# Kernel tuning notes

Hardware: AMD Instinct MI355X
Metric: run time of the kernel (lower is better)

## Reference

```python
import jax, jax.numpy as jnp
import numpy as np

N_NODE = 50000
N_EDGE = 800000
NODE_DIM, EDGE_DIM = 3, 4


def _relu(x):
    return jnp.maximum(x, 0)


def setup_inputs() -> dict:
    key = jax.random.key(0)
    ks = jax.random.split(key, 32)
    ki = iter(range(32))

    def w(shape):
        fan = shape[0]
        return (jax.random.normal(ks[next(ki)], shape, jnp.float32) / np.float32(np.sqrt(fan)))

    def b(n):
        return jnp.zeros((n,), jnp.float32)

    inp = {
        'nodes': jax.random.normal(ks[next(ki)], (N_NODE, NODE_DIM), jnp.float32),
        'edges': jax.random.normal(ks[next(ki)], (N_EDGE, EDGE_DIM), jnp.float32),
        'senders': jax.random.randint(ks[next(ki)], (N_EDGE,), 0, N_NODE, jnp.int32),
        'receivers': jax.random.randint(ks[next(ki)], (N_EDGE,), 0, N_NODE, jnp.int32),
        # psi1 encoder: [10 -> 256 -> 256 -> 128], relu after every layer (act_final=True)
        'mw0': w((NODE_DIM * 2 + EDGE_DIM, 256)), 'mb0': b(256),
        'mw1': w((256, 256)), 'mb1': b(256),
        'mw2': w((256, 128)), 'mb2': b(128),
        # psi2 attention: [128 -> 128 -> 128 -> 1], no final act
        'aw0': w((128, 128)), 'ab0': b(128),
        'aw1': w((128, 128)), 'ab1': b(128),
        'aw2': w((128, 1)), 'ab2': b(1),
        # psi3 value: [128 -> 256 -> 128], relu after every layer
        'vw0': w((128, 256)), 'vb0': b(256),
        'vw1': w((256, 128)), 'vb1': b(128),
        # psi4 decoder: [128 -> 256 -> 256 -> 1], no final act
        'uw0': w((128, 256)), 'ub0': b(256),
        'uw1': w((256, 256)), 'ub1': b(256),
        'uw2': w((256, 1)), 'ub2': b(1),
    }
    return inp


def reference(nodes, edges, senders, receivers,
              mw0, mb0, mw1, mb1, mw2, mb2,
              aw0, ab0, aw1, ab1, aw2, ab2,
              vw0, vb0, vw1, vb1,
              uw0, ub0, uw1, ub1, uw2, ub2):
    n_node = nodes.shape[0]
    # gather endpoint features and concat with edge features: (E, 2*node_dim+edge_dim)
    z = jnp.concatenate([nodes[senders], nodes[receivers], edges], axis=-1)
    # psi1 encoder (act_final=True)
    q = _relu(_relu(_relu(z @ mw0 + mb0) @ mw1 + mb1) @ mw2 + mb2)  # (E,128)
    # psi2 attention logits (no final act)
    w = (_relu(_relu(q @ aw0 + ab0) @ aw1 + ab1) @ aw2 + ab2)[:, 0]  # (E,)
    # segment softmax over receivers (matches torch scatter_reduce amax with -1e9 init)
    m = jax.ops.segment_max(w, receivers, num_segments=n_node)
    m = jnp.maximum(m, jnp.float32(-1e9))
    ex = jnp.exp(w - m[receivers])
    s = jax.ops.segment_sum(ex, receivers, num_segments=n_node)
    attn = ex / (s[receivers] + 1e-12)  # (E,)
    # psi3 value (act_final=True)
    v = _relu(_relu(q @ vw0 + vb0) @ vw1 + vb1)  # (E,128)
    # attention-weighted scatter-add aggregation to receiver nodes
    aggr = jax.ops.segment_sum(attn[:, None] * v, receivers, num_segments=n_node)  # (N,128)
    # psi4 decoder (no final act)
    out = _relu(_relu(aggr @ uw0 + ub0) @ uw1 + ub1) @ uw2 + ub2  # (N,1)
    return out
```

## Files before the change

kernel.cpp:

```cpp
#include <hip/hip_runtime.h>
#include <stdint.h>

#define NN_NODE 50000
#define NN_EDGE 800000

typedef _Float16 f16;
typedef _Float16 f16x2 __attribute__((ext_vector_type(2)));
typedef _Float16 f16x4 __attribute__((ext_vector_type(4)));
typedef _Float16 f16x8 __attribute__((ext_vector_type(8)));
typedef float f32x4 __attribute__((ext_vector_type(4)));

#define WT_MW0   0
#define WT_MW1   8192
#define WT_MW2   73728
#define WT_AW0   106496
#define WT_AW1   122880
#define WT_VW0   139264
#define WT_VW1   172032
#define WT_UW0   204800
#define WT_UW1   237568
#define WT_TOTAL 303104

#define V_OFF      606208ull
#define WL_OFF     205406208ull
#define CNT_OFF    208606208ull
#define BASE_OFF   208806208ull
#define AGGR_OFF   209006208ull

__device__ __forceinline__ int swz(int row, int col) {
    return row * 256 + ((((col >> 3) ^ (row & 7))) << 3) + (col & 7);
}

template<int K, int N, int KN, int EPI>
__device__ __forceinline__ void mlayer(const f16* in, int inoff,
        const f16* __restrict__ wt, const float* __restrict__ bias,
        f16* out, int outoff,
        f16x8* bf0, const f16* __restrict__ wtn, f16x8* bfn,
        const float* __restrict__ aw2, float* lpart,
        f16* __restrict__ vout, const int* sposp, int tid)
{
    const int wave = tid >> 6;
    const int lane = tid & 63;
    const int l15  = lane & 15;
    const int quad = lane >> 4;
    constexpr int NKS  = K >> 5;
    constexpr int NKH  = (NKS > 4) ? 4 : NKS;
    constexpr int NH   = NKS / NKH;
    constexpr int NCT  = N >> 4;
    constexpr int ITC  = NCT / 4;
    constexpr int NKNH = (KN >= 128) ? 4 : (KN >> 5);

    f32x4 acc[ITC][4];
#pragma unroll
    for (int i = 0; i < ITC; ++i)
#pragma unroll
        for (int ms = 0; ms < 4; ++ms)
            acc[i][ms] = (f32x4){0.f, 0.f, 0.f, 0.f};

    int sposv[4];
    if constexpr (EPI == 2) {
#pragma unroll
        for (int ms = 0; ms < 4; ++ms) sposv[ms] = sposp[ms * 16 + l15];
    }

    f16x8 bfl[2][NKH];

#pragma unroll
    for (int h = 0; h < NH; ++h) {
        if (h == 0) {
#pragma unroll
            for (int ks = 0; ks < NKH; ++ks) bfl[0][ks] = bf0[ks];
        } else {
            const f16* wrow = wt + (size_t)(wave * 16 + l15) * K + h * NKH * 32 + quad * 8;
#pragma unroll
            for (int ks = 0; ks < NKH; ++ks)
                bfl[0][ks] = *(const f16x8*)(wrow + ks * 32);
        }

        f16x8 af[4][NKH];
#pragma unroll
        for (int ms = 0; ms < 4; ++ms)
#pragma unroll
            for (int ks = 0; ks < NKH; ++ks)
                af[ms][ks] = *(const f16x8*)(in + swz(ms * 16 + l15,
                                    inoff + (h * NKH + ks) * 32 + quad * 8));
#pragma unroll
        for (int ms = 0; ms < 4; ++ms)
#pragma unroll
            for (int ks = 0; ks < NKH; ++ks)
                asm volatile("" : "+v"(af[ms][ks]));

        if constexpr (KN > 0) {
            if (h == NH - 1) {
                const f16* wrow = wtn + (size_t)(wave * 16 + l15) * KN + quad * 8;
#pragma unroll
                for (int ks = 0; ks < NKNH; ++ks)
                    bfn[ks] = *(const f16x8*)(wrow + ks * 32);
            }
        }

#pragma unroll
        for (int i = 0; i < ITC; ++i) {
            const int ct = wave + i * 4;
            if (i + 1 < ITC) {
                const f16* wrow2 = wt + (size_t)((ct + 4) * 16 + l15) * K + h * NKH * 32 + quad * 8;
#pragma unroll
                for (int ks = 0; ks < NKH; ++ks)
                    bfl[(i + 1) & 1][ks] = *(const f16x8*)(wrow2 + ks * 32);
            }
#pragma unroll
            for (int ms = 0; ms < 4; ++ms)
#pragma unroll
                for (int ks = 0; ks < NKH; ++ks)
                    acc[i][ms] = __builtin_amdgcn_mfma_f32_16x16x32_f16(
                        bfl[i & 1][ks], af[ms][ks], acc[i][ms], 0, 0, 0);
        }
    }

    float preg[4];
    if constexpr (EPI == 1) {
#pragma unroll
        for (int ms = 0; ms < 4; ++ms) preg[ms] = 0.f;
    }
#pragma unroll
    for (int i = 0; i < ITC; ++i) {
        const int ct = wave + i * 4;
        const int f0 = ct * 16 + quad * 4;
        const float4 bv = *(const float4*)(bias + f0);
        float4 awv;
        if constexpr (EPI == 1) awv = *(const float4*)(aw2 + f0);
#pragma unroll
        for (int ms = 0; ms < 4; ++ms) {
            if constexpr (EPI == 0) {
                f16x4 o;
                o[0] = (f16)fmaxf(acc[i][ms][0] + bv.x, 0.f);
                o[1] = (f16)fmaxf(acc[i][ms][1] + bv.y, 0.f);
                o[2] = (f16)fmaxf(acc[i][ms][2] + bv.z, 0.f);
                o[3] = (f16)fmaxf(acc[i][ms][3] + bv.w, 0.f);
                *(f16x4*)(out + swz(ms * 16 + l15, outoff + f0)) = o;
            } else if constexpr (EPI == 1) {
                preg[ms] += fmaxf(acc[i][ms][0] + bv.x, 0.f) * awv.x
                          + fmaxf(acc[i][ms][1] + bv.y, 0.f) * awv.y
                          + fmaxf(acc[i][ms][2] + bv.z, 0.f) * awv.z
                          + fmaxf(acc[i][ms][3] + bv.w, 0.f) * awv.w;
            } else {
                f16x4 o;
                o[0] = (f16)fmaxf(acc[i][ms][0] + bv.x, 0.f);
                o[1] = (f16)fmaxf(acc[i][ms][1] + bv.y, 0.f);
                o[2] = (f16)fmaxf(acc[i][ms][2] + bv.z, 0.f);
                o[3] = (f16)fmaxf(acc[i][ms][3] + bv.w, 0.f);
                *(f16x4*)(vout + (size_t)sposv[ms] * 128 + f0) = o;
            }
        }
    }
    if constexpr (EPI == 1) {
#pragma unroll
        for (int ms = 0; ms < 4; ++ms) {
            float r = preg[ms];
            r += __shfl_xor(r, 16);
            r += __shfl_xor(r, 32);
            if (quad == 0) lpart[wave * 64 + ms * 16 + l15] = r;
        }
    }
}

template<int K, int N>
__device__ __forceinline__ void mfma_layer_basic(const f16* in, int inoff,
        const f16* __restrict__ wt, const float* __restrict__ bias,
        f16* out, int outoff, int tid)
{
    const int wave = tid >> 6;
    const int lane = tid & 63;
    const int l15  = lane & 15;
    const int quad = lane >> 4;
    constexpr int NCT = N >> 4;
    constexpr int NKS = K >> 5;
    f16x8 af[4][NKS];
#pragma unroll
    for (int ms = 0; ms < 4; ++ms)
#pragma unroll
        for (int ks = 0; ks < NKS; ++ks)
            af[ms][ks] = *(const f16x8*)(in + swz(ms * 16 + l15, inoff + ks * 32 + quad * 8));
#pragma unroll 1
    for (int ct = wave; ct < NCT; ct += 4) {
        f16x8 bf[NKS];
        const f16* wrow = wt + (size_t)(ct * 16 + l15) * K + quad * 8;
#pragma unroll
        for (int ks = 0; ks < NKS; ++ks) bf[ks] = *(const f16x8*)(wrow + ks * 32);
        const int f0 = ct * 16 + quad * 4;
        const float4 bv = *(const float4*)(bias + f0);
#pragma unroll
        for (int ms = 0; ms < 4; ++ms) {
            f32x4 acc = {0.f, 0.f, 0.f, 0.f};
#pragma unroll
            for (int ks = 0; ks < NKS; ++ks)
                acc = __builtin_amdgcn_mfma_f32_16x16x32_f16(bf[ks], af[ms][ks], acc, 0, 0, 0);
            f16x4 o;
            o[0] = (f16)fmaxf(acc[0] + bv.x, 0.f);
            o[1] = (f16)fmaxf(acc[1] + bv.y, 0.f);
            o[2] = (f16)fmaxf(acc[2] + bv.z, 0.f);
            o[3] = (f16)fmaxf(acc[3] + bv.w, 0.f);
            *(f16x4*)(out + swz(ms * 16 + l15, outoff + f0)) = o;
        }
    }
}

struct WSeg { const float* src; int K, N, Kpad, dstOff; };
struct WSegs { WSeg s[9]; };

__global__ void prep_kernel(WSegs segs, f16* __restrict__ wt) {
    int idx = blockIdx.x * 256 + threadIdx.x;
    if (idx >= WT_TOTAL) return;
    int off = idx;
#pragma unroll
    for (int i = 0; i < 9; ++i) {
        int sz = segs.s[i].N * segs.s[i].Kpad;
        if (off < sz) {
            int n = off / segs.s[i].Kpad;
            int k = off - n * segs.s[i].Kpad;
            f16 val = (f16)0.f;
            if (k < segs.s[i].K) val = (f16)segs.s[i].src[k * segs.s[i].N + n];
            wt[segs.s[i].dstOff + off] = val;
            return;
        }
        off -= sz;
    }
}

__global__ void hist_kernel(const int* __restrict__ receivers, int* __restrict__ cnt) {
    int e = blockIdx.x * 256 + threadIdx.x;
    atomicAdd(&cnt[receivers[e]], 1);
}

__global__ __launch_bounds__(1024) void scan_kernel(int* __restrict__ cnt, int* __restrict__ base) {
    __shared__ int psum[1024];
    const int tid = threadIdx.x;
    const int CH = (NN_NODE + 1023) / 1024;
    const int lo = tid * CH;
    const int hi = min(lo + CH, NN_NODE);
    int s = 0;
    for (int i = lo; i < hi; ++i) s += cnt[i];
    psum[tid] = s;
    __syncthreads();
    for (int d = 1; d < 1024; d <<= 1) {
        int v = (tid >= d) ? psum[tid - d] : 0;
        __syncthreads();
        psum[tid] += v;
        __syncthreads();
    }
    int run = psum[tid] - s;
    for (int i = lo; i < hi; ++i) {
        int c = cnt[i];
        base[i] = run;
        cnt[i] = run;
        run += c;
    }
}

__global__ __launch_bounds__(256, 2) void edge_kernel(
        const float* __restrict__ nodes, const float* __restrict__ edges,
        const int* __restrict__ senders, const int* __restrict__ receivers,
        const f16* __restrict__ wt,
        const float* __restrict__ mb0, const float* __restrict__ mb1, const float* __restrict__ mb2,
        const float* __restrict__ ab0, const float* __restrict__ ab1,
        const float* __restrict__ aw2, const float* __restrict__ ab2,
        const float* __restrict__ vb0, const float* __restrict__ vb1,
        f16* __restrict__ vout, float* __restrict__ wlog, int* __restrict__ cursor)
{
    __shared__ f16 ldsbuf[2 * 64 * 256];
    __shared__ int spos[64];
    __shared__ float lpart[256];
    f16* bufA = ldsbuf;
    f16* bufB = ldsbuf + 64 * 256;
    const int tid = threadIdx.x;
    const int e0 = blockIdx.x * 64;
    const int wave = tid >> 6;
    const int lane = tid & 63;
    const int l15  = lane & 15;
    const int quad = lane >> 4;

    f16x8 bfA[4], bfB[4];

    {
        const f16* wrow = wt + WT_MW0 + (size_t)(wave * 16 + l15) * 32 + quad * 8;
        bfA[0] = *(const f16x8*)wrow;
    }

    {
        const int e = tid & 63, c = tid >> 6;
        f16x8 zv = {(f16)0.f,(f16)0.f,(f16)0.f,(f16)0.f,(f16)0.f,(f16)0.f,(f16)0.f,(f16)0.f};
        if (c == 0) {
            int s = senders[e0 + e];
            int r = receivers[e0 + e];
            const float2 ev = *(const float2*)(edges + (size_t)(e0 + e) * 4);
            zv[0] = (f16)nodes[s * 3 + 0]; zv[1] = (f16)nodes[s * 3 + 1]; zv[2] = (f16)nodes[s * 3 + 2];
            zv[3] = (f16)nodes[r * 3 + 0]; zv[4] = (f16)nodes[r * 3 + 1]; zv[5] = (f16)nodes[r * 3 + 2];
            zv[6] = (f16)ev.x; zv[7] = (f16)ev.y;
        } else if (c == 1) {
            const float2 ev = *(const float2*)(edges + (size_t)(e0 + e) * 4 + 2);
            zv[0] = (f16)ev.x; zv[1] = (f16)ev.y;
        }
        *(f16x8*)(bufA + e * 256 + ((c ^ (e & 7)) << 3)) = zv;
    }
    __syncthreads();

    mlayer< 32, 256, 256, 0>(bufA, 0, wt + WT_MW0, mb0, bufB, 0, bfA, wt + WT_MW1, bfB,
                             nullptr, nullptr, nullptr, nullptr, tid);
    __syncthreads();
    mlayer<256, 256, 256, 0>(bufB, 0, wt + WT_MW1, mb1, bufA, 0, bfB, wt + WT_MW2, bfA,
                             nullptr, nullptr, nullptr, nullptr, tid);
    __syncthreads();
    mlayer<256, 128, 128, 0>(bufA, 0, wt + WT_MW2, mb2, bufB, 0, bfA, wt + WT_AW0, bfB,
                             nullptr, nullptr, nullptr, nullptr, tid);
    __syncthreads();
    mlayer<128, 128, 128, 0>(bufB, 0, wt + WT_AW0, ab0, bufA, 0, bfB, wt + WT_AW1, bfA,
                             nullptr, nullptr, nullptr, nullptr, tid);
    __syncthreads();
    mlayer<128, 128, 128, 1>(bufA, 0, wt + WT_AW1, ab1, nullptr, 0, bfA, wt + WT_VW0, bfB,
                             aw2, lpart, nullptr, nullptr, tid);
    __syncthreads();

    if (tid < 64) {
        float wv = lpart[tid] + lpart[64 + tid] + lpart[128 + tid] + lpart[192 + tid] + ab2[0];
        int r = receivers[e0 + tid];
        int pos = atomicAdd(&cursor[r], 1);
        spos[tid] = pos;
        wlog[pos] = wv;
    }
    mlayer<128, 256, 256, 0>(bufB, 0, wt + WT_VW0, vb0, bufA, 0, bfB, wt + WT_VW1, bfA,
                             nullptr, nullptr, nullptr, nullptr, tid);
    __syncthreads();
    mlayer<256, 128, 0, 2>(bufA, 0, wt + WT_VW1, vb1, nullptr, 0, bfA, nullptr, nullptr,
                           nullptr, nullptr, vout, spos, tid);
}

__global__ __launch_bounds__(256) void aggregate_kernel(
        const float* __restrict__ wlog, const f16* __restrict__ v,
        const int* __restrict__ base, float* __restrict__ aggr)
{
    const int tid = threadIdx.x;
    const int n = blockIdx.x * 4 + (tid >> 6);
    const int lane = tid & 63;
    const int st = base[n];
    const int en = (n == NN_NODE - 1) ? NN_EDGE : base[n + 1];

    float mx = -1e9f;
    for (int i = st + lane; i < en; i += 64) mx = fmaxf(mx, wlog[i]);
#pragma unroll
    for (int d = 1; d < 64; d <<= 1) mx = fmaxf(mx, __shfl_xor(mx, d));

    float sm = 0.f;
    for (int i = st + lane; i < en; i += 64) sm += __expf(wlog[i] - mx);
#pragma unroll
    for (int d = 1; d < 64; d <<= 1) sm += __shfl_xor(sm, d);
    const float inv = 1.f / (sm + 1e-12f);

    float acc0 = 0.f, acc1 = 0.f;
    const f16* vp = v + (size_t)st * 128 + lane * 2;
    for (int i = st; i < en; ++i, vp += 128) {
        float attn = __expf(wlog[i] - mx) * inv;
        f16x2 vv = *(const f16x2*)vp;
        acc0 += attn * (float)vv[0];
        acc1 += attn * (float)vv[1];
    }
    float2 o; o.x = acc0; o.y = acc1;
    *(float2*)(aggr + (size_t)n * 128 + lane * 2) = o;
}

__global__ __launch_bounds__(256, 2) void node_kernel(
        const float* __restrict__ aggr, const f16* __restrict__ wt,
        const float* __restrict__ ub0, const float* __restrict__ ub1,
        const float* __restrict__ uw2, const float* __restrict__ ub2,
        float* __restrict__ out)
{
    __shared__ f16 ldsbuf[2 * 64 * 256];
    f16* bufA = ldsbuf;
    f16* bufB = ldsbuf + 64 * 256;
    const int tid = threadIdx.x;
    const int n0 = blockIdx.x * 64;
    {
        int row = tid >> 2, j = tid & 3;
        int n = n0 + row;
        if (n < NN_NODE) {
            const float4* src = (const float4*)(aggr + (size_t)n * 128 + j * 32);
#pragma unroll
            for (int i = 0; i < 8; ++i) {
                float4 t4 = src[i];
                int c = j * 32 + i * 4;
                bufA[swz(row, c + 0)] = (f16)t4.x;
                bufA[swz(row, c + 1)] = (f16)t4.y;
                bufA[swz(row, c + 2)] = (f16)t4.z;
                bufA[swz(row, c + 3)] = (f16)t4.w;
            }
        } else {
#pragma unroll
            for (int i = 0; i < 32; ++i) bufA[swz(row, j * 32 + i)] = (f16)0.f;
        }
    }
    __syncthreads();
    mfma_layer_basic<128, 256>(bufA, 0, wt + WT_UW0, ub0, bufB, 0, tid); __syncthreads();
    mfma_layer_basic<256, 256>(bufB, 0, wt + WT_UW1, ub1, bufA, 0, tid); __syncthreads();
    {
        int e = tid >> 2, part = tid & 3;
        float sum = 0.f;
        for (int c = part * 64; c < part * 64 + 64; ++c)
            sum += (float)bufA[swz(e, c)] * uw2[c];
        sum += __shfl_down(sum, 2);
        sum += __shfl_down(sum, 1);
        int n = n0 + e;
        if (part == 0 && n < NN_NODE) out[n] = sum + ub2[0];
    }
}

extern "C" void kernel_launch(void* const* d_in, const int* in_sizes, int n_in,
                              void* d_out, int out_size, void* d_ws, size_t ws_size,
                              hipStream_t stream)
{
    const float* nodes     = (const float*)d_in[0];
    const float* edges     = (const float*)d_in[1];
    const int*   senders   = (const int*)d_in[2];
    const int*   receivers = (const int*)d_in[3];
    const float* mw0 = (const float*)d_in[4];  const float* mb0 = (const float*)d_in[5];
    const float* mw1 = (const float*)d_in[6];  const float* mb1 = (const float*)d_in[7];
    const float* mw2 = (const float*)d_in[8];  const float* mb2 = (const float*)d_in[9];
    const float* aw0 = (const float*)d_in[10]; const float* ab0 = (const float*)d_in[11];
    const float* aw1 = (const float*)d_in[12]; const float* ab1 = (const float*)d_in[13];
    const float* aw2 = (const float*)d_in[14]; const float* ab2 = (const float*)d_in[15];
    const float* vw0 = (const float*)d_in[16]; const float* vb0 = (const float*)d_in[17];
    const float* vw1 = (const float*)d_in[18]; const float* vb1 = (const float*)d_in[19];
    const float* uw0 = (const float*)d_in[20]; const float* ub0 = (const float*)d_in[21];
    const float* uw1 = (const float*)d_in[22]; const float* ub1 = (const float*)d_in[23];
    const float* uw2 = (const float*)d_in[24]; const float* ub2 = (const float*)d_in[25];

    char* ws = (char*)d_ws;
    f16*   wt   = (f16*)ws;
    f16*   vbuf = (f16*)(ws + V_OFF);
    float* wlog = (float*)(ws + WL_OFF);
    int*   cnt  = (int*)(ws + CNT_OFF);
    int*   base = (int*)(ws + BASE_OFF);
    float* aggr = (float*)(ws + AGGR_OFF);
    float* out  = (float*)d_out;

    hipMemsetAsync(cnt, 0, NN_NODE * sizeof(int), stream);

    WSegs segs = {{
        { mw0,  10, 256,  32, WT_MW0 },
        { mw1, 256, 256, 256, WT_MW1 },
        { mw2, 256, 128, 256, WT_MW2 },
        { aw0, 128, 128, 128, WT_AW0 },
        { aw1, 128, 128, 128, WT_AW1 },
        { vw0, 128, 256, 128, WT_VW0 },
        { vw1, 256, 128, 256, WT_VW1 },
        { uw0, 128, 256, 128, WT_UW0 },
        { uw1, 256, 256, 256, WT_UW1 },
    }};
    prep_kernel<<<(WT_TOTAL + 255) / 256, 256, 0, stream>>>(segs, wt);

    hist_kernel<<<NN_EDGE / 256, 256, 0, stream>>>(receivers, cnt);
    scan_kernel<<<1, 1024, 0, stream>>>(cnt, base);

    edge_kernel<<<NN_EDGE / 64, 256, 0, stream>>>(nodes, edges, senders, receivers, wt,
        mb0, mb1, mb2, ab0, ab1, aw2, ab2, vb0, vb1, vbuf, wlog, cnt);

    aggregate_kernel<<<NN_NODE / 4, 256, 0, stream>>>(wlog, vbuf, base, aggr);

    node_kernel<<<(NN_NODE + 63) / 64, 256, 0, stream>>>(aggr, wt, ub0, ub1, uw2, ub2, out);
}
```

Before: 973.7 us.

## Deepen weight-fragment prefetch to three stages across flattened MLP layer tiles

```diff
diff --git a/kernel.cpp b/kernel.cpp
--- a/kernel.cpp
+++ b/kernel.cpp
@@ -35,7 +35,7 @@
 __device__ __forceinline__ void mlayer(const f16* in, int inoff,
         const f16* __restrict__ wt, const float* __restrict__ bias,
         f16* out, int outoff,
-        f16x8* bf0, const f16* __restrict__ wtn, f16x8* bfn,
+        f16x8 (&bf0)[2][4], const f16* __restrict__ wtn, f16x8 (&bfn)[2][4],
         const float* __restrict__ aw2, float* lpart,
         f16* __restrict__ vout, const int* sposp, int tid)
 {
@@ -48,6 +48,8 @@
     constexpr int NH   = NKS / NKH;
     constexpr int NCT  = N >> 4;
     constexpr int ITC  = NCT / 4;
+    constexpr int NT   = NH * ITC;
+    constexpr int PD   = (NT >= 3) ? 3 : 2;
     constexpr int NKNH = (KN >= 128) ? 4 : (KN >> 5);
 
     f32x4 acc[ITC][4];
@@ -63,57 +65,68 @@
         for (int ms = 0; ms < 4; ++ms) sposv[ms] = sposp[ms * 16 + l15];
     }
 
-    f16x8 bfl[2][NKH];
-
-#pragma unroll
-    for (int h = 0; h < NH; ++h) {
-        if (h == 0) {
-#pragma unroll
-            for (int ks = 0; ks < NKH; ++ks) bfl[0][ks] = bf0[ks];
-        } else {
-            const f16* wrow = wt + (size_t)(wave * 16 + l15) * K + h * NKH * 32 + quad * 8;
+    f16x8 af[4][NKH];
+    f16x8 bfl[3][NKH];
+
+#pragma unroll
+    for (int ks = 0; ks < NKH; ++ks) bfl[0][ks] = bf0[0][ks];
+#pragma unroll
+    for (int ks = 0; ks < NKH; ++ks) bfl[1][ks] = bf0[1][ks];
+    if constexpr (NT > 2) {
+        constexpr int h2 = 2 / ITC, i2 = 2 % ITC;
+        const f16* w2 = wt + (size_t)((wave + i2 * 4) * 16 + l15) * K + h2 * NKH * 32 + quad * 8;
+#pragma unroll
+        for (int ks = 0; ks < NKH; ++ks) bfl[2][ks] = *(const f16x8*)(w2 + ks * 32);
+    }
+
+#pragma unroll
+    for (int ms = 0; ms < 4; ++ms)
+#pragma unroll
+        for (int ks = 0; ks < NKH; ++ks)
+            af[ms][ks] = *(const f16x8*)(in + swz(ms * 16 + l15,
+                                inoff + ks * 32 + quad * 8));
+#pragma unroll
+    for (int ms = 0; ms < 4; ++ms)
+#pragma unroll
+        for (int ks = 0; ks < NKH; ++ks)
+            asm volatile("" : "+v"(af[ms][ks]));
+
+#pragma unroll
+    for (int s = 0; s < NT; ++s) {
+        const int is = s % ITC;
+        if (NH == 2 && s == ITC) {
+#pragma unroll
+            for (int ms = 0; ms < 4; ++ms)
+#pragma unroll
+                for (int ks = 0; ks < NKH; ++ks)
+                    af[ms][ks] = *(const f16x8*)(in + swz(ms * 16 + l15,
+                                        inoff + (NKH + ks) * 32 + quad * 8));
+#pragma unroll
+            for (int ms = 0; ms < 4; ++ms)
+#pragma unroll
+                for (int ks = 0; ks < NKH; ++ks)
+                    asm volatile("" : "+v"(af[ms][ks]));
+        }
+#pragma unroll
+        for (int ms = 0; ms < 4; ++ms)
 #pragma unroll
             for (int ks = 0; ks < NKH; ++ks)
-                bfl[0][ks] = *(const f16x8*)(wrow + ks * 32);
-        }
-
-        f16x8 af[4][NKH];
-#pragma unroll
-        for (int ms = 0; ms < 4; ++ms)
+                acc[is][ms] = __builtin_amdgcn_mfma_f32_16x16x32_f16(
+                    bfl[s % 3][ks], af[ms][ks], acc[is][ms], 0, 0, 0);
+        if (s + PD < NT) {
+            const int t = s + PD, ht = t / ITC, it = t % ITC;
+            const f16* wr = wt + (size_t)((wave + it * 4) * 16 + l15) * K + ht * NKH * 32 + quad * 8;
 #pragma unroll
             for (int ks = 0; ks < NKH; ++ks)
-                af[ms][ks] = *(const f16x8*)(in + swz(ms * 16 + l15,
-                                    inoff + (h * NKH + ks) * 32 + quad * 8));
-#pragma unroll
-        for (int ms = 0; ms < 4; ++ms)
-#pragma unroll
-            for (int ks = 0; ks < NKH; ++ks)
-                asm volatile("" : "+v"(af[ms][ks]));
-
-        if constexpr (KN > 0) {
-            if (h == NH - 1) {
-                const f16* wrow = wtn + (size_t)(wave * 16 + l15) * KN + quad * 8;
+                bfl[t % 3][ks] = *(const f16x8*)(wr + ks * 32);
+        } else if constexpr (KN > 0) {
+            const int j = s + PD - NT;
+            if (j < 2) {
+                const f16* wr = wtn + (size_t)((wave + j * 4) * 16 + l15) * KN + quad * 8;
 #pragma unroll
                 for (int ks = 0; ks < NKNH; ++ks)
-                    bfn[ks] = *(const f16x8*)(wrow + ks * 32);
+                    bfn[j][ks] = *(const f16x8*)(wr + ks * 32);
             }
-        }
-
-#pragma unroll
-        for (int i = 0; i < ITC; ++i) {
-            const int ct = wave + i * 4;
-            if (i + 1 < ITC) {
-                const f16* wrow2 = wt + (size_t)((ct + 4) * 16 + l15) * K + h * NKH * 32 + quad * 8;
-#pragma unroll
-                for (int ks = 0; ks < NKH; ++ks)
-                    bfl[(i + 1) & 1][ks] = *(const f16x8*)(wrow2 + ks * 32);
-            }
-#pragma unroll
-            for (int ms = 0; ms < 4; ++ms)
-#pragma unroll
-                for (int ks = 0; ks < NKH; ++ks)
-                    acc[i][ms] = __builtin_amdgcn_mfma_f32_16x16x32_f16(
-                        bfl[i & 1][ks], af[ms][ks], acc[i][ms], 0, 0, 0);
         }
     }
 
@@ -279,11 +292,12 @@
     const int l15  = lane & 15;
     const int quad = lane >> 4;
 
-    f16x8 bfA[4], bfB[4];
+    f16x8 bfA[2][4], bfB[2][4];
 
     {
         const f16* wrow = wt + WT_MW0 + (size_t)(wave * 16 + l15) * 32 + quad * 8;
-        bfA[0] = *(const f16x8*)wrow;
+        bfA[0][0] = *(const f16x8*)wrow;
+        bfA[1][0] = *(const f16x8*)(wrow + 64 * 32);
     }
 
     {
@@ -330,7 +344,7 @@
     mlayer<128, 256, 256, 0>(bufB, 0, wt + WT_VW0, vb0, bufA, 0, bfB, wt + WT_VW1, bfA,
                              nullptr, nullptr, nullptr, nullptr, tid);
     __syncthreads();
-    mlayer<256, 128, 0, 2>(bufA, 0, wt + WT_VW1, vb1, nullptr, 0, bfA, nullptr, nullptr,
+    mlayer<256, 128, 0, 2>(bufA, 0, wt + WT_VW1, vb1, nullptr, 0, bfA, nullptr, bfB,
                            nullptr, nullptr, vout, spos, tid);
 }
 
```

Result: no change. 969.9 us (-0.4%).
